# Optimization experiments

Measured on AMD Instinct MI355X. Metric: run time of the kernel, lower is better.

Reference implementation:

```python
import jax, jax.numpy as jnp
import numpy as np

CAPS = 16          # num_capsules
DIM = 16           # capsule_dim
NUM_ROUTING = 3
L2_EPS = 1e-12     # tf.nn.l2_normalize epsilon


def setup_inputs() -> dict:
    key = jax.random.key(0)
    k1, k2 = jax.random.split(key)
    inputs = jax.random.normal(k1, (16, 64, 64, 128), dtype=jnp.float32)
    # Conv2D kernel, HWIO layout, fan-in scaled like glorot-ish init
    kernel = jax.random.normal(k2, (3, 3, 128, CAPS * DIM), dtype=jnp.float32) * 0.03
    bias = jnp.zeros((CAPS * DIM,), dtype=jnp.float32)
    return {"inputs": inputs, "kernel": kernel, "bias": bias}


def reference(inputs, kernel, bias):
    # Conv2D(caps*dim, 3x3, padding='same', activation='relu'), channels_last
    x = jax.lax.conv_general_dilated(
        inputs, kernel, window_strides=(1, 1), padding="SAME",
        dimension_numbers=("NHWC", "HWIO", "NHWC"))
    x = jax.nn.relu(x + bias)
    B, H, W, _ = x.shape
    x = x.reshape(B, H * W, CAPS, DIM)            # (B, N, C, D)
    b = jnp.zeros((B, H * W, CAPS), dtype=x.dtype)
    v = None
    for _ in range(NUM_ROUTING):
        c = jax.nn.softmax(b, axis=-1)             # over capsules
        s = jnp.einsum("bnc,bncd->bcd", c, x)      # weighted sum over spatial
        # tf.nn.l2_normalize along last axis
        v = s * jax.lax.rsqrt(jnp.maximum(jnp.sum(s * s, axis=-1, keepdims=True), L2_EPS))
        b = b + jnp.einsum("bncd,bcd->bnc", x, v)  # agreement update
    # tile v over spatial dims: (B,1,1,C*D) -> (B,H,W,C*D)
    out = jnp.broadcast_to(v.reshape(B, 1, 1, CAPS * DIM), (B, H, W, CAPS * DIM))
    return out
```

## Files before the change

### kernel.cpp

```cpp
#include <hip/hip_runtime.h>
#include <hip/hip_bf16.h>

typedef unsigned short u16;
typedef unsigned int   u32;

typedef __bf16 bf16x8 __attribute__((ext_vector_type(8)));
typedef float  f32x4  __attribute__((ext_vector_type(4)));

#define GLDS(gp, lp) __builtin_amdgcn_global_load_lds( \
    (const __attribute__((address_space(1))) void*)(gp), \
    (__attribute__((address_space(3))) void*)(lp), 16, 0, 0)

__device__ __forceinline__ u16 f2b(float f) {
    __hip_bfloat16 h = __float2bfloat16(f);
    u16 u; __builtin_memcpy(&u, &h, 2); return u;
}
__device__ __forceinline__ float blo(u32 u) { return __uint_as_float(u << 16); }
__device__ __forceinline__ float bhi(u32 u) { return __uint_as_float(u & 0xffff0000u); }

__global__ void k_prep(const float* __restrict__ in, const float* __restrict__ wk,
                       u16* __restrict__ pad, u16* __restrict__ BF,
                       float* __restrict__ stats) {
    int bx = blockIdx.x, tid = threadIdx.x;
    if (bx < 4356) {
        int idx = bx * 256 + tid;
        int e0  = idx * 8;
        int ch  = e0 & 127;
        int rest = e0 >> 7;
        int pw = rest % 66;
        int r2 = rest / 66;
        int ph = r2 % 66;
        int b  = r2 / 66;
        u16 ov[8];
        if (ph >= 1 && ph <= 64 && pw >= 1 && pw <= 64) {
            const float* src = in + (((b * 64 + (ph - 1)) * 64 + (pw - 1)) * 128 + ch);
            const float4* s4 = (const float4*)src;
            float4 f0 = s4[0], f1 = s4[1];
            ov[0]=f2b(f0.x); ov[1]=f2b(f0.y); ov[2]=f2b(f0.z); ov[3]=f2b(f0.w);
            ov[4]=f2b(f1.x); ov[5]=f2b(f1.y); ov[6]=f2b(f1.z); ov[7]=f2b(f1.w);
        } else {
            #pragma unroll
            for (int j = 0; j < 8; ++j) ov[j] = 0;
        }
        uint4 w; __builtin_memcpy(&w, ov, 16);
        *(uint4*)(pad + e0) = w;
    } else if (bx < 5508) {
        int t = (bx - 4356) * 256 + tid;
        int j  = t & 7;
        int n  = (t >> 3) & 255;
        int q  = (t >> 11) & 3;
        int kk = (t >> 13) & 3;
        int p  = t >> 15;
        BF[t] = f2b(wk[(p * 128 + kk * 32 + q * 8 + j) * 256 + n]);
    } else {
        stats[(bx - 5508) * 256 + tid] = 0.f;
    }
}

__launch_bounds__(256, 2)
__global__ void k_conv(const u16* __restrict__ Ap, const u16* __restrict__ BF,
                       const float* __restrict__ bias,
                       u16* __restrict__ X, float* __restrict__ s0) {
    __shared__ u16 ldsA[12672];
    const int t = threadIdx.x;
    const int lane = t & 63, wid = t >> 6;
    const int q = lane >> 4, l15 = lane & 15;
    const int bb = blockIdx.x >> 6;
    const int h  = blockIdx.x & 63;
    const int wn0 = wid << 6;

#define STAGE(S) { \
    const int sb0 = wid * 396; \
    _Pragma("unroll") for (int i = 0; i < 6; ++i) { \
        int sb = sb0 + i * 64; \
        int slot = sb + lane; \
        int pr = slot / 528; int rem = slot - pr * 528; \
        int wp = rem >> 3, cs = rem & 7; \
        int gc = (S) * 8 + (cs ^ (wp & 7)); \
        const u16* g = Ap + ((((bb * 66 + h + pr) * 66 + wp) << 7) + (gc << 3)); \
        GLDS(g, (char*)ldsA + sb * 16); \
    } \
    { int sb = sb0 + 384; \
      if (lane < 12) { \
        int slot = sb + lane; \
        int pr = slot / 528; int rem = slot - pr * 528; \
        int wp = rem >> 3, cs = rem & 7; \
        int gc = (S) * 8 + (cs ^ (wp & 7)); \
        const u16* g = Ap + ((((bb * 66 + h + pr) * 66 + wp) << 7) + (gc << 3)); \
        GLDS(g, (char*)ldsA + sb * 16); \
      } } }

#define LOADB(B, P, S) { \
    _Pragma("unroll") for (int kk = 0; kk < 2; ++kk) \
    _Pragma("unroll") for (int ni = 0; ni < 4; ++ni) \
        B[kk * 4 + ni] = *(const bf16x8*)(BFl + (P) * 32768 + \
                                          ((S) * 2 + kk) * 8192 + ni * 128); }

#define COMPP(B, DH, DW) { \
    _Pragma("unroll") for (int kk = 0; kk < 2; ++kk) { \
        bf16x8 af[4]; \
        _Pragma("unroll") for (int mi = 0; mi < 4; ++mi) { \
            int wp = mi * 16 + l15 + (DW); \
            int swz = (kk * 4 + q) ^ (wp & 7); \
            af[mi] = *(const bf16x8*)((const char*)ldsA + \
                (((DH) * 528 + wp * 8 + swz) << 4)); \
        } \
        _Pragma("unroll") for (int mi = 0; mi < 4; ++mi) \
        _Pragma("unroll") for (int ni = 0; ni < 4; ++ni) \
            acc[mi][ni] = __builtin_amdgcn_mfma_f32_16x16x32_bf16( \
                af[mi], B[kk * 4 + ni], acc[mi][ni], 0, 0, 0); } }

    const u16* BFl = BF + (q * 2048 + (wn0 + l15) * 8);

    f32x4 zero = {0.f, 0.f, 0.f, 0.f};
    f32x4 acc[4][4];
    #pragma unroll
    for (int mi = 0; mi < 4; ++mi)
        #pragma unroll
        for (int ni = 0; ni < 4; ++ni) acc[mi][ni] = zero;

    bf16x8 B0[8], B1[8];

    STAGE(0);
    __syncthreads();
    LOADB(B0, 0, 0);
    LOADB(B1, 1, 0); COMPP(B0, 0, 0);
    LOADB(B0, 2, 0); COMPP(B1, 0, 1);
    LOADB(B1, 3, 0); COMPP(B0, 0, 2);
    LOADB(B0, 4, 0); COMPP(B1, 1, 0);
    LOADB(B1, 5, 0); COMPP(B0, 1, 1);
    LOADB(B0, 6, 0); COMPP(B1, 1, 2);
    LOADB(B1, 7, 0); COMPP(B0, 2, 0);
    LOADB(B0, 8, 0); COMPP(B1, 2, 1);
    COMPP(B0, 2, 2);
    __syncthreads();

    STAGE(1);
    __syncthreads();
    LOADB(B0, 0, 1);
    LOADB(B1, 1, 1); COMPP(B0, 0, 0);
    LOADB(B0, 2, 1); COMPP(B1, 0, 1);
    LOADB(B1, 3, 1); COMPP(B0, 0, 2);
    LOADB(B0, 4, 1); COMPP(B1, 1, 0);
    LOADB(B1, 5, 1); COMPP(B0, 1, 1);
    LOADB(B0, 6, 1); COMPP(B1, 1, 2);
    LOADB(B1, 7, 1); COMPP(B0, 2, 0);
    LOADB(B0, 8, 1); COMPP(B1, 2, 1);
    COMPP(B0, 2, 2);

    float bv[4];
    #pragma unroll
    for (int ni = 0; ni < 4; ++ni) bv[ni] = bias[wn0 + ni * 16 + l15];
    float colsum[4] = {0.f, 0.f, 0.f, 0.f};
    u16* xrow = X + (((bb << 12) + (h << 6) + q * 4) * 256) + wn0 + l15;
    #pragma unroll
    for (int mi = 0; mi < 4; ++mi) {
        #pragma unroll
        for (int rr = 0; rr < 4; ++rr) {
            u16* xp = xrow + (mi * 16 + rr) * 256;
            #pragma unroll
            for (int ni = 0; ni < 4; ++ni) {
                float v = acc[mi][ni][rr] + bv[ni];
                v = v > 0.f ? v : 0.f;
                xp[ni * 16] = f2b(v);
                colsum[ni] += v;
            }
        }
    }
    #pragma unroll
    for (int ni = 0; ni < 4; ++ni) {
        float c = colsum[ni];
        c += __shfl_xor(c, 16);
        c += __shfl_xor(c, 32);
        if (lane < 16) atomicAdd(&s0[bb * 256 + wn0 + ni * 16 + l15], c);
    }
#undef STAGE
#undef LOADB
#undef COMPP
}

__global__ void k_pass(const u16* __restrict__ X, const float* __restrict__ Sa,
                       const float* __restrict__ Sb, float* __restrict__ Sout,
                       int use2) {
    __shared__ float v1s[256], v2s[256];
    __shared__ float red[4096];
    int t = threadIdx.x, b = blockIdx.y, chunk = blockIdx.x;
    {
        float sa = Sa[b * 256 + t];
        float ss = sa * sa;
        #pragma unroll
        for (int off = 1; off < 16; off <<= 1) ss += __shfl_xor(ss, off);
        ss = ss < 1e-12f ? 1e-12f : ss;
        v1s[t] = sa / sqrtf(ss);
        if (use2) {
            float sb = Sb[b * 256 + t];
            float s2 = sb * sb;
            #pragma unroll
            for (int off = 1; off < 16; off <<= 1) s2 += __shfl_xor(s2, off);
            s2 = s2 < 1e-12f ? 1e-12f : s2;
            v2s[t] = sb / sqrtf(s2);
        } else {
            v2s[t] = 0.f;
        }
    }
    __syncthreads();
    int c = t & 15, nl = t >> 4;
    float acc[16];
    #pragma unroll
    for (int d = 0; d < 16; ++d) acc[d] = 0.f;

    const u16* xbase = X + ((b << 12) + chunk * 64 + nl) * 256 + c * 16;
    uint4 p0 = ((const uint4*)xbase)[0];
    uint4 p1 = ((const uint4*)xbase)[1];
    for (int r = 0; r < 4; ++r) {
        uint4 a0 = p0, a1 = p1;
        if (r < 3) {
            const u16* np = xbase + (r + 1) * 16 * 256;
            p0 = ((const uint4*)np)[0];
            p1 = ((const uint4*)np)[1];
        }
        u32 us[8] = {a0.x, a0.y, a0.z, a0.w, a1.x, a1.y, a1.z, a1.w};
        float xf[16];
        #pragma unroll
        for (int j = 0; j < 8; ++j) { xf[2*j] = blo(us[j]); xf[2*j+1] = bhi(us[j]); }
        float d1 = 0.f, d2 = 0.f;
        #pragma unroll
        for (int d = 0; d < 16; ++d) {
            d1 += xf[d] * v1s[c * 16 + d];
            d2 += xf[d] * v2s[c * 16 + d];
        }
        float bvv = use2 ? (d1 + d2) : d1;
        float e = __expf(bvv);
        float sm = e;
        #pragma unroll
        for (int off = 1; off < 16; off <<= 1) sm += __shfl_xor(sm, off);
        float w = e / sm;
        #pragma unroll
        for (int d = 0; d < 16; ++d) acc[d] += w * xf[d];
    }
    #pragma unroll
    for (int d = 0; d < 16; ++d) red[t * 16 + d] = acc[d];
    __syncthreads();
    int c2 = t >> 4, d2i = t & 15;
    float tot = 0.f;
    #pragma unroll
    for (int n2 = 0; n2 < 16; ++n2) tot += red[(n2 * 16 + c2) * 16 + d2i];
    atomicAdd(&Sout[b * 256 + c2 * 16 + d2i], tot);
}

__global__ void k_bcast(const float* __restrict__ S, float* __restrict__ Out) {
    __shared__ float4 vls[64];
    int t = threadIdx.x, bx = blockIdx.x, b = blockIdx.y;
    float s = S[b * 256 + t];
    float ss = s * s;
    #pragma unroll
    for (int off = 1; off < 16; off <<= 1) ss += __shfl_xor(ss, off);
    ss = ss < 1e-12f ? 1e-12f : ss;
    ((float*)vls)[t] = s / sqrtf(ss);
    __syncthreads();
    float4* o = (float4*)Out + (long)b * 262144 + bx * 8192;
    #pragma unroll
    for (int j = 0; j < 32; ++j) {
        int idx = j * 256 + t;
        o[idx] = vls[idx & 63];
    }
}

extern "C" void kernel_launch(void* const* d_in, const int* in_sizes, int n_in,
                              void* d_out, int out_size, void* d_ws, size_t ws_size,
                              hipStream_t stream) {
    const float* in   = (const float*)d_in[0];
    const float* wk   = (const float*)d_in[1];
    const float* bias = (const float*)d_in[2];
    float* out = (float*)d_out;
    char* ws = (char*)d_ws;

    const size_t OFF_PAD = 0;
    const size_t OFF_BF  = 17842176;
    const size_t OFF_X   = 18432000;
    const size_t OFF_ST  = 51986432;
    const size_t NEEDED  = OFF_ST + 3 * 16384;
    if (ws_size < NEEDED) return;

    u16* pad = (u16*)(ws + OFF_PAD);
    u16* BF  = (u16*)(ws + OFF_BF);
    u16* X   = (u16*)(ws + OFF_X);
    float* s0 = (float*)(ws + OFF_ST);
    float* s2 = s0 + 4096;
    float* s3 = s2 + 4096;

    k_prep <<<5556, 256, 0, stream>>>(in, wk, pad, BF, s0);
    k_conv <<<1024, 256, 0, stream>>>(pad, BF, bias, X, s0);
    k_pass <<<dim3(64, 16), 256, 0, stream>>>(X, s0, s0, s2, 0);
    k_pass <<<dim3(64, 16), 256, 0, stream>>>(X, s0, s2, s3, 1);
    k_bcast<<<dim3(32, 16), 256, 0, stream>>>(s3, out);
}
```

Baseline: 163.5 us.

## Compute two output rows per conv block to reuse weight fragments

Each conv block now computes two image rows (128 output pixels) instead of one. It stages four padded input rows in LDS and doubles the MFMA accumulator tile, so every B-weight fragment loaded from global memory is reused across twice as many rows. B fragment loads are also software-pipelined ahead of the LDS staging and across the two channel stages. The cost is twice as many accumulator registers and half as many blocks (512), which may lower occupancy and leave CUs underused on a 256-CU part.

```diff
diff --git a/kernel.cpp b/kernel.cpp
--- a/kernel.cpp
+++ b/kernel.cpp
@@ -61,32 +61,32 @@
 __global__ void k_conv(const u16* __restrict__ Ap, const u16* __restrict__ BF,
                        const float* __restrict__ bias,
                        u16* __restrict__ X, float* __restrict__ s0) {
-    __shared__ u16 ldsA[12672];
+    __shared__ u16 ldsA[16896];
     const int t = threadIdx.x;
     const int lane = t & 63, wid = t >> 6;
     const int q = lane >> 4, l15 = lane & 15;
-    const int bb = blockIdx.x >> 6;
-    const int h  = blockIdx.x & 63;
+    const int bb = blockIdx.x >> 5;
+    const int h0 = (blockIdx.x & 31) << 1;
     const int wn0 = wid << 6;
 
 #define STAGE(S) { \
-    const int sb0 = wid * 396; \
-    _Pragma("unroll") for (int i = 0; i < 6; ++i) { \
+    const int sb0 = wid * 528; \
+    _Pragma("unroll") for (int i = 0; i < 8; ++i) { \
         int sb = sb0 + i * 64; \
         int slot = sb + lane; \
         int pr = slot / 528; int rem = slot - pr * 528; \
         int wp = rem >> 3, cs = rem & 7; \
         int gc = (S) * 8 + (cs ^ (wp & 7)); \
-        const u16* g = Ap + ((((bb * 66 + h + pr) * 66 + wp) << 7) + (gc << 3)); \
+        const u16* g = Ap + ((((bb * 66 + h0 + pr) * 66 + wp) << 7) + (gc << 3)); \
         GLDS(g, (char*)ldsA + sb * 16); \
     } \
-    { int sb = sb0 + 384; \
-      if (lane < 12) { \
+    { int sb = sb0 + 512; \
+      if (lane < 16) { \
         int slot = sb + lane; \
         int pr = slot / 528; int rem = slot - pr * 528; \
         int wp = rem >> 3, cs = rem & 7; \
         int gc = (S) * 8 + (cs ^ (wp & 7)); \
-        const u16* g = Ap + ((((bb * 66 + h + pr) * 66 + wp) << 7) + (gc << 3)); \
+        const u16* g = Ap + ((((bb * 66 + h0 + pr) * 66 + wp) << 7) + (gc << 3)); \
         GLDS(g, (char*)ldsA + sb * 16); \
       } } }
 
@@ -98,14 +98,15 @@
 
 #define COMPP(B, DH, DW) { \
     _Pragma("unroll") for (int kk = 0; kk < 2; ++kk) { \
-        bf16x8 af[4]; \
-        _Pragma("unroll") for (int mi = 0; mi < 4; ++mi) { \
-            int wp = mi * 16 + l15 + (DW); \
+        bf16x8 af[8]; \
+        _Pragma("unroll") for (int mi = 0; mi < 8; ++mi) { \
+            int wp = ((mi & 3) << 4) + l15 + (DW); \
+            int pr = (mi >> 2) + (DH); \
             int swz = (kk * 4 + q) ^ (wp & 7); \
             af[mi] = *(const bf16x8*)((const char*)ldsA + \
-                (((DH) * 528 + wp * 8 + swz) << 4)); \
+                ((pr * 528 + wp * 8 + swz) << 4)); \
         } \
-        _Pragma("unroll") for (int mi = 0; mi < 4; ++mi) \
+        _Pragma("unroll") for (int mi = 0; mi < 8; ++mi) \
         _Pragma("unroll") for (int ni = 0; ni < 4; ++ni) \
             acc[mi][ni] = __builtin_amdgcn_mfma_f32_16x16x32_bf16( \
                 af[mi], B[kk * 4 + ni], acc[mi][ni], 0, 0, 0); } }
@@ -113,51 +114,53 @@
     const u16* BFl = BF + (q * 2048 + (wn0 + l15) * 8);
 
     f32x4 zero = {0.f, 0.f, 0.f, 0.f};
-    f32x4 acc[4][4];
-    #pragma unroll
-    for (int mi = 0; mi < 4; ++mi)
+    f32x4 acc[8][4];
+    #pragma unroll
+    for (int mi = 0; mi < 8; ++mi)
         #pragma unroll
         for (int ni = 0; ni < 4; ++ni) acc[mi][ni] = zero;
 
     bf16x8 B0[8], B1[8];
 
+    LOADB(B0, 0, 0);
+    LOADB(B1, 1, 0);
     STAGE(0);
     __syncthreads();
-    LOADB(B0, 0, 0);
-    LOADB(B1, 1, 0); COMPP(B0, 0, 0);
-    LOADB(B0, 2, 0); COMPP(B1, 0, 1);
-    LOADB(B1, 3, 0); COMPP(B0, 0, 2);
-    LOADB(B0, 4, 0); COMPP(B1, 1, 0);
-    LOADB(B1, 5, 0); COMPP(B0, 1, 1);
-    LOADB(B0, 6, 0); COMPP(B1, 1, 2);
-    LOADB(B1, 7, 0); COMPP(B0, 2, 0);
-    LOADB(B0, 8, 0); COMPP(B1, 2, 1);
-    COMPP(B0, 2, 2);
+    COMPP(B0, 0, 0); LOADB(B0, 2, 0);
+    COMPP(B1, 0, 1); LOADB(B1, 3, 0);
+    COMPP(B0, 0, 2); LOADB(B0, 4, 0);
+    COMPP(B1, 1, 0); LOADB(B1, 5, 0);
+    COMPP(B0, 1, 1); LOADB(B0, 6, 0);
+    COMPP(B1, 1, 2); LOADB(B1, 7, 0);
+    COMPP(B0, 2, 0); LOADB(B0, 8, 0);
+    COMPP(B1, 2, 1); LOADB(B1, 0, 1);
+    COMPP(B0, 2, 2); LOADB(B0, 1, 1);
     __syncthreads();
 
     STAGE(1);
     __syncthreads();
-    LOADB(B0, 0, 1);
-    LOADB(B1, 1, 1); COMPP(B0, 0, 0);
-    LOADB(B0, 2, 1); COMPP(B1, 0, 1);
-    LOADB(B1, 3, 1); COMPP(B0, 0, 2);
-    LOADB(B0, 4, 1); COMPP(B1, 1, 0);
-    LOADB(B1, 5, 1); COMPP(B0, 1, 1);
-    LOADB(B0, 6, 1); COMPP(B1, 1, 2);
-    LOADB(B1, 7, 1); COMPP(B0, 2, 0);
-    LOADB(B0, 8, 1); COMPP(B1, 2, 1);
-    COMPP(B0, 2, 2);
+    COMPP(B1, 0, 0); LOADB(B1, 2, 1);
+    COMPP(B0, 0, 1); LOADB(B0, 3, 1);
+    COMPP(B1, 0, 2); LOADB(B1, 4, 1);
+    COMPP(B0, 1, 0); LOADB(B0, 5, 1);
+    COMPP(B1, 1, 1); LOADB(B1, 6, 1);
+    COMPP(B0, 1, 2); LOADB(B0, 7, 1);
+    COMPP(B1, 2, 0); LOADB(B1, 8, 1);
+    COMPP(B0, 2, 1);
+    COMPP(B1, 2, 2);
 
     float bv[4];
     #pragma unroll
     for (int ni = 0; ni < 4; ++ni) bv[ni] = bias[wn0 + ni * 16 + l15];
     float colsum[4] = {0.f, 0.f, 0.f, 0.f};
-    u16* xrow = X + (((bb << 12) + (h << 6) + q * 4) * 256) + wn0 + l15;
-    #pragma unroll
-    for (int mi = 0; mi < 4; ++mi) {
+    #pragma unroll
+    for (int mi = 0; mi < 8; ++mi) {
+        int hrow = h0 + (mi >> 2);
+        u16* xr = X + (((bb << 12) + (hrow << 6) + ((mi & 3) << 4) + q * 4) * 256)
+                    + wn0 + l15;
         #pragma unroll
         for (int rr = 0; rr < 4; ++rr) {
-            u16* xp = xrow + (mi * 16 + rr) * 256;
+            u16* xp = xr + rr * 256;
             #pragma unroll
             for (int ni = 0; ni < 4; ++ni) {
                 float v = acc[mi][ni][rr] + bv[ni];
@@ -290,7 +293,7 @@
     float* s3 = s2 + 4096;
 
     k_prep <<<5556, 256, 0, stream>>>(in, wk, pad, BF, s0);
-    k_conv <<<1024, 256, 0, stream>>>(pad, BF, bias, X, s0);
+    k_conv <<<512, 256, 0, stream>>>(pad, BF, bias, X, s0);
     k_pass <<<dim3(64, 16), 256, 0, stream>>>(X, s0, s0, s2, 0);
     k_pass <<<dim3(64, 16), 256, 0, stream>>>(X, s0, s2, s3, 1);
     k_bcast<<<dim3(32, 16), 256, 0, stream>>>(s3, out);
```

New measurement: 200.7 us. +22.8%, slower.

## Fuse routing passes and broadcast into one persistent kernel with grid barriers

Applied to the files above, without the earlier changes.

Replaces the two routing-pass launches and the broadcast launch with one 512-block kernel. The stages are separated by software grid barriers built on an atomic counter, and the extra k_prep block presumably zeroes that counter. The aim is to remove two kernel launch gaps and their tail effects. In exchange each block handles twice as many spatial rows, and the code relies on all 512 blocks being resident at once for the spin barrier to make progress.

```diff
diff --git a/kernel.cpp b/kernel.cpp
--- a/kernel.cpp
+++ b/kernel.cpp
@@ -179,91 +179,115 @@
 #undef COMPP
 }
 
-__global__ void k_pass(const u16* __restrict__ X, const float* __restrict__ Sa,
-                       const float* __restrict__ Sb, float* __restrict__ Sout,
-                       int use2) {
+__device__ __forceinline__ void gridbar(u32* ctr, u32 nblk) {
+    __syncthreads();
+    if (threadIdx.x == 0) {
+        __threadfence();
+        __hip_atomic_fetch_add(ctr, 1u, __ATOMIC_RELEASE, __HIP_MEMORY_SCOPE_AGENT);
+        u32 v; unsigned long g = 0;
+        do {
+            v = __hip_atomic_load(ctr, __ATOMIC_ACQUIRE, __HIP_MEMORY_SCOPE_AGENT);
+        } while (v < nblk && ++g < (1ul << 31));
+    }
+    __syncthreads();
+}
+
+__launch_bounds__(256, 4)
+__global__ void k_route(const u16* __restrict__ X, const float* __restrict__ s0,
+                        float* __restrict__ s2, float* __restrict__ s3,
+                        u32* __restrict__ bar, float* __restrict__ out) {
     __shared__ float v1s[256], v2s[256];
     __shared__ float red[4096];
-    int t = threadIdx.x, b = blockIdx.y, chunk = blockIdx.x;
+    const int t = threadIdx.x, bx = blockIdx.x;
+    const int b = bx >> 5, chunk = bx & 31;
+    const int c = t & 15, nl = t >> 4;
+
+#define PASS_BODY(SA_EXPR, SB_EXPR, USE2, SOUT) { \
+    { \
+        float sa = (SA_EXPR); \
+        float ss = sa * sa; \
+        _Pragma("unroll") \
+        for (int off = 1; off < 16; off <<= 1) ss += __shfl_xor(ss, off); \
+        ss = ss < 1e-12f ? 1e-12f : ss; \
+        v1s[t] = sa / sqrtf(ss); \
+        if (USE2) { \
+            float sb = (SB_EXPR); \
+            float s2v = sb * sb; \
+            _Pragma("unroll") \
+            for (int off = 1; off < 16; off <<= 1) s2v += __shfl_xor(s2v, off); \
+            s2v = s2v < 1e-12f ? 1e-12f : s2v; \
+            v2s[t] = sb / sqrtf(s2v); \
+        } else { v2s[t] = 0.f; } \
+    } \
+    __syncthreads(); \
+    float acc[16]; \
+    _Pragma("unroll") for (int d = 0; d < 16; ++d) acc[d] = 0.f; \
+    const u16* xbase = X + ((b << 12) + chunk * 128 + nl) * 256 + c * 16; \
+    uint4 p0 = ((const uint4*)xbase)[0]; \
+    uint4 p1 = ((const uint4*)xbase)[1]; \
+    for (int r = 0; r < 8; ++r) { \
+        uint4 a0 = p0, a1 = p1; \
+        if (r < 7) { \
+            const u16* np = xbase + (r + 1) * 16 * 256; \
+            p0 = ((const uint4*)np)[0]; \
+            p1 = ((const uint4*)np)[1]; \
+        } \
+        u32 us[8] = {a0.x, a0.y, a0.z, a0.w, a1.x, a1.y, a1.z, a1.w}; \
+        float xf[16]; \
+        _Pragma("unroll") \
+        for (int j = 0; j < 8; ++j) { xf[2*j] = blo(us[j]); xf[2*j+1] = bhi(us[j]); } \
+        float d1 = 0.f, d2 = 0.f; \
+        _Pragma("unroll") \
+        for (int d = 0; d < 16; ++d) { \
+            d1 += xf[d] * v1s[c * 16 + d]; \
+            d2 += xf[d] * v2s[c * 16 + d]; \
+        } \
+        float bvv = (USE2) ? (d1 + d2) : d1; \
+        float e = __expf(bvv); \
+        float sm = e; \
+        _Pragma("unroll") \
+        for (int off = 1; off < 16; off <<= 1) sm += __shfl_xor(sm, off); \
+        float w = e / sm; \
+        _Pragma("unroll") \
+        for (int d = 0; d < 16; ++d) acc[d] += w * xf[d]; \
+    } \
+    _Pragma("unroll") \
+    for (int d = 0; d < 16; ++d) red[t * 16 + d] = acc[d]; \
+    __syncthreads(); \
+    { \
+        int c2 = t >> 4, d2i = t & 15; \
+        float tot = 0.f; \
+        _Pragma("unroll") \
+        for (int n2 = 0; n2 < 16; ++n2) tot += red[(n2 * 16 + c2) * 16 + d2i]; \
+        atomicAdd(&(SOUT)[b * 256 + c2 * 16 + d2i], tot); \
+    } }
+
+    PASS_BODY(s0[b * 256 + t], 0.f, 0, s2)
+    gridbar(&bar[0], 512);
+
+    PASS_BODY(s0[b * 256 + t],
+              __hip_atomic_load(&s2[b * 256 + t], __ATOMIC_RELAXED,
+                                __HIP_MEMORY_SCOPE_AGENT), 1, s3)
+    gridbar(&bar[1], 512);
+
     {
-        float sa = Sa[b * 256 + t];
-        float ss = sa * sa;
+        float s = __hip_atomic_load(&s3[b * 256 + t], __ATOMIC_RELAXED,
+                                    __HIP_MEMORY_SCOPE_AGENT);
+        float ss = s * s;
         #pragma unroll
         for (int off = 1; off < 16; off <<= 1) ss += __shfl_xor(ss, off);
         ss = ss < 1e-12f ? 1e-12f : ss;
-        v1s[t] = sa / sqrtf(ss);
-        if (use2) {
-            float sb = Sb[b * 256 + t];
-            float s2 = sb * sb;
-            #pragma unroll
-            for (int off = 1; off < 16; off <<= 1) s2 += __shfl_xor(s2, off);
-            s2 = s2 < 1e-12f ? 1e-12f : s2;
-            v2s[t] = sb / sqrtf(s2);
-        } else {
-            v2s[t] = 0.f;
-        }
-    }
-    __syncthreads();
-    int c = t & 15, nl = t >> 4;
-    float acc[16];
-    #pragma unroll
-    for (int d = 0; d < 16; ++d) acc[d] = 0.f;
-
-    const u16* xbase = X + ((b << 12) + chunk * 64 + nl) * 256 + c * 16;
-    uint4 p0 = ((const uint4*)xbase)[0];
-    uint4 p1 = ((const uint4*)xbase)[1];
-    for (int r = 0; r < 4; ++r) {
-        uint4 a0 = p0, a1 = p1;
-        if (r < 3) {
-            const u16* np = xbase + (r + 1) * 16 * 256;
-            p0 = ((const uint4*)np)[0];
-            p1 = ((const uint4*)np)[1];
-        }
-        u32 us[8] = {a0.x, a0.y, a0.z, a0.w, a1.x, a1.y, a1.z, a1.w};
-        float xf[16];
-        #pragma unroll
-        for (int j = 0; j < 8; ++j) { xf[2*j] = blo(us[j]); xf[2*j+1] = bhi(us[j]); }
-        float d1 = 0.f, d2 = 0.f;
-        #pragma unroll
-        for (int d = 0; d < 16; ++d) {
-            d1 += xf[d] * v1s[c * 16 + d];
-            d2 += xf[d] * v2s[c * 16 + d];
-        }
-        float bvv = use2 ? (d1 + d2) : d1;
-        float e = __expf(bvv);
-        float sm = e;
-        #pragma unroll
-        for (int off = 1; off < 16; off <<= 1) sm += __shfl_xor(sm, off);
-        float w = e / sm;
-        #pragma unroll
-        for (int d = 0; d < 16; ++d) acc[d] += w * xf[d];
-    }
-    #pragma unroll
-    for (int d = 0; d < 16; ++d) red[t * 16 + d] = acc[d];
-    __syncthreads();
-    int c2 = t >> 4, d2i = t & 15;
-    float tot = 0.f;
-    #pragma unroll
-    for (int n2 = 0; n2 < 16; ++n2) tot += red[(n2 * 16 + c2) * 16 + d2i];
-    atomicAdd(&Sout[b * 256 + c2 * 16 + d2i], tot);
-}
-
-__global__ void k_bcast(const float* __restrict__ S, float* __restrict__ Out) {
-    __shared__ float4 vls[64];
-    int t = threadIdx.x, bx = blockIdx.x, b = blockIdx.y;
-    float s = S[b * 256 + t];
-    float ss = s * s;
-    #pragma unroll
-    for (int off = 1; off < 16; off <<= 1) ss += __shfl_xor(ss, off);
-    ss = ss < 1e-12f ? 1e-12f : ss;
-    ((float*)vls)[t] = s / sqrtf(ss);
-    __syncthreads();
-    float4* o = (float4*)Out + (long)b * 262144 + bx * 8192;
+        v1s[t] = s / sqrtf(ss);
+    }
+    __syncthreads();
+    const float4* vls = (const float4*)v1s;
+    float4* o = (float4*)out + (long)b * 262144 + chunk * 8192;
     #pragma unroll
     for (int j = 0; j < 32; ++j) {
         int idx = j * 256 + t;
         o[idx] = vls[idx & 63];
     }
+#undef PASS_BODY
 }
 
 extern "C" void kernel_launch(void* const* d_in, const int* in_sizes, int n_in,
@@ -279,7 +303,7 @@
     const size_t OFF_BF  = 17842176;
     const size_t OFF_X   = 18432000;
     const size_t OFF_ST  = 51986432;
-    const size_t NEEDED  = OFF_ST + 3 * 16384;
+    const size_t NEEDED  = OFF_ST + 12544 * 4;
     if (ws_size < NEEDED) return;
 
     u16* pad = (u16*)(ws + OFF_PAD);
@@ -288,10 +312,9 @@
     float* s0 = (float*)(ws + OFF_ST);
     float* s2 = s0 + 4096;
     float* s3 = s2 + 4096;
-
-    k_prep <<<5556, 256, 0, stream>>>(in, wk, pad, BF, s0);
+    u32*  bar = (u32*)(s3 + 4096);
+
+    k_prep <<<5557, 256, 0, stream>>>(in, wk, pad, BF, s0);
     k_conv <<<1024, 256, 0, stream>>>(pad, BF, bias, X, s0);
-    k_pass <<<dim3(64, 16), 256, 0, stream>>>(X, s0, s0, s2, 0);
-    k_pass <<<dim3(64, 16), 256, 0, stream>>>(X, s0, s2, s3, 1);
-    k_bcast<<<dim3(32, 16), 256, 0, stream>>>(s3, out);
-}
+    k_route<<<512,  256, 0, stream>>>(X, s0, s2, s3, bar, out);
+}
```

After: 291.9 us. 78.5% more time.
